# Kernel tuning notes

Hardware: AMD Instinct MI355X
Metric: run time of the kernel (lower is better)

## Reference

```python
import jax, jax.numpy as jnp
import numpy as np

N = 100_000      # n_nodes
E = 1_000_000    # n_edges (avg degree 10)
DIN = 64
DOUT = 64


def setup_inputs() -> dict:
    key = jax.random.key(0)
    k1, k2, k3, k4 = jax.random.split(key, 4)
    x = jax.random.normal(k1, (N, DIN), dtype=jnp.float32)
    edge_index = jax.random.randint(k2, (2, E), 0, N, dtype=jnp.int32)
    # GCNConv linear weight (glorot-ish scale) and bias
    W = jax.random.normal(k3, (DIN, DOUT), dtype=jnp.float32) * (1.0 / np.sqrt(DIN))
    b = jax.random.normal(k4, (DOUT,), dtype=jnp.float32) * 0.01
    return {"x": x, "edge_index": edge_index, "W": W, "b": b}


def reference(x, edge_index, W, b):
    n = x.shape[0]
    # linear transform first (PyG GCNConv: x = self.lin(x))
    h = x @ W  # [N, DOUT]
    # add self-loops
    loop = jnp.arange(n, dtype=edge_index.dtype)
    row = jnp.concatenate([edge_index[0], loop])  # source j
    col = jnp.concatenate([edge_index[1], loop])  # target i
    # symmetric normalization: deg computed on target index (PyG gcn_norm)
    deg = jax.ops.segment_sum(jnp.ones(row.shape[0], dtype=h.dtype), col, num_segments=n)
    dinv = jnp.where(deg > 0, jax.lax.rsqrt(deg), 0.0)
    norm = dinv[row] * dinv[col]  # [E+N]
    # gather source features, scale, scatter-add to targets
    out = jax.ops.segment_sum(norm[:, None] * h[row], col, num_segments=n)
    out = out + b
    # dropout is identity in eval mode; act = relu
    return jax.nn.relu(out)
```

## Files before the change

kernel.cpp:

```cpp
#include <hip/hip_runtime.h>
#include <hip/hip_bf16.h>

#define F 64
#define BK 64
#define CAP 1024
#define ECAP 1024
#define KMAX 1600
#define PA_BLOCKS 512

typedef __attribute__((ext_vector_type(8))) short bf16x8;
typedef __attribute__((ext_vector_type(4))) float f32x4;

static __device__ inline short f2bf_bits(float f) {
    union { __hip_bfloat16 b; short s; } cv;
    cv.b = __float2bfloat16(f);
    return cv.s;
}

__global__ void __launch_bounds__(256)
k1_kernel(const float* __restrict__ x, const float* __restrict__ W,
          __hip_bfloat16* __restrict__ h,
          const int* __restrict__ row, const int* __restrict__ col,
          int* __restrict__ bcursor, unsigned* __restrict__ bin,
          int n, int e, int ngemm, int K, int chunk) {
    __shared__ int smem[2 * KMAX];
    int tid = threadIdx.x;

    if ((int)blockIdx.x < ngemm) {
        short* Wb = (short*)smem;
        for (int i = tid; i < F * F; i += 256) Wb[i] = f2bf_bits(W[i]);
        __syncthreads();
        int lane = tid & 63;
        int wv = tid >> 6;
        int quad = lane >> 4;
        int l16 = lane & 15;

        bf16x8 bfr[2][4];
#pragma unroll
        for (int ks = 0; ks < 2; ++ks)
#pragma unroll
            for (int nb = 0; nb < 4; ++nb) {
                bf16x8 f;
#pragma unroll
                for (int j = 0; j < 8; ++j)
                    f[j] = Wb[(ks * 32 + quad * 8 + j) * F + nb * 16 + l16];
                bfr[ks][nb] = f;
            }

        int blockbase = blockIdx.x * 128;
#pragma unroll
        for (int mt = 0; mt < 2; ++mt) {
            int trow = blockbase + (wv * 2 + mt) * 16;
            int ar = trow + l16;
            bf16x8 af0, af1;
            if (ar < n) {
                const float* xr = x + (size_t)ar * F + quad * 8;
                float4 v0 = ((const float4*)xr)[0];
                float4 v1 = ((const float4*)xr)[1];
                float4 v2 = ((const float4*)(xr + 32))[0];
                float4 v3 = ((const float4*)(xr + 32))[1];
                af0[0] = f2bf_bits(v0.x); af0[1] = f2bf_bits(v0.y);
                af0[2] = f2bf_bits(v0.z); af0[3] = f2bf_bits(v0.w);
                af0[4] = f2bf_bits(v1.x); af0[5] = f2bf_bits(v1.y);
                af0[6] = f2bf_bits(v1.z); af0[7] = f2bf_bits(v1.w);
                af1[0] = f2bf_bits(v2.x); af1[1] = f2bf_bits(v2.y);
                af1[2] = f2bf_bits(v2.z); af1[3] = f2bf_bits(v2.w);
                af1[4] = f2bf_bits(v3.x); af1[5] = f2bf_bits(v3.y);
                af1[6] = f2bf_bits(v3.z); af1[7] = f2bf_bits(v3.w);
            } else {
                af0 = (bf16x8)0; af1 = (bf16x8)0;
            }
            f32x4 acc[4];
#pragma unroll
            for (int nb = 0; nb < 4; ++nb) {
                acc[nb] = (f32x4)0.f;
                acc[nb] = __builtin_amdgcn_mfma_f32_16x16x32_bf16(af0, bfr[0][nb], acc[nb], 0, 0, 0);
                acc[nb] = __builtin_amdgcn_mfma_f32_16x16x32_bf16(af1, bfr[1][nb], acc[nb], 0, 0, 0);
            }
#pragma unroll
            for (int nb = 0; nb < 4; ++nb)
#pragma unroll
                for (int r = 0; r < 4; ++r) {
                    int grow = trow + quad * 4 + r;
                    if (grow < n)
                        h[(size_t)grow * F + nb * 16 + l16] = __float2bfloat16(acc[nb][r]);
                }
        }
    } else {
        int* lh = smem;
        int* lbase = smem + KMAX;
        int pb = blockIdx.x - ngemm;
        int s = pb * chunk;
        int lim = min(s + chunk, e);
        for (int i = tid; i < K; i += 256) lh[i] = 0;
        __syncthreads();
        for (int i = s + tid; i < lim; i += 256) atomicAdd(&lh[col[i] >> 6], 1);
        __syncthreads();
        for (int i = tid; i < K; i += 256) {
            int c = lh[i];
            lbase[i] = c ? atomicAdd(&bcursor[i], c) : 0;
            lh[i] = 0;
        }
        __syncthreads();
        for (int i = s + tid; i < lim; i += 256) {
            int d = col[i];
            int bkt = d >> 6;
            int off = lbase[bkt] + atomicAdd(&lh[bkt], 1);
            if (off < CAP)
                bin[(size_t)bkt * CAP + off] = ((unsigned)row[i] << 6) | ((unsigned)d & 63u);
        }
    }
}

__global__ void __launch_bounds__(256)
dinv_kernel(const unsigned* __restrict__ bin, const int* __restrict__ bcursor,
            float* __restrict__ dinv, int n) {
    __shared__ int lcnt[BK];
    int tid = threadIdx.x;
    int b = blockIdx.x;
    int s = b * CAP;
    int cnt = min(bcursor[b], ECAP);
    if (tid < BK) lcnt[tid] = 0;
    __syncthreads();
    for (int p = tid; p < cnt; p += 256) atomicAdd(&lcnt[bin[s + p] & 63u], 1);
    __syncthreads();
    if (tid < BK) {
        int node = (b << 6) + tid;
        if (node < n) dinv[node] = rsqrtf((float)(lcnt[tid] + 1));
    }
}

__global__ void __launch_bounds__(256)
gather_kernel(const unsigned* __restrict__ bin, const int* __restrict__ bcursor,
              const float* __restrict__ dinv, const __hip_bfloat16* __restrict__ h,
              const float* __restrict__ bias, float* __restrict__ out, int n) {
    __shared__ unsigned ebuf[ECAP];
    __shared__ uint2 sent[ECAP];
    __shared__ int lcnt[BK];
    __shared__ int sstart[BK];
    __shared__ int lcur[BK];
    __shared__ int sc[BK];
    __shared__ float sdinv[BK];
    int tid = threadIdx.x;
    int b = blockIdx.x;
    int base = b << 6;
    int s = b * CAP;
    int cnt = min(bcursor[b], ECAP);

    if (tid < BK) lcnt[tid] = 0;
    __syncthreads();
    for (int p = tid; p < cnt; p += 256) {
        unsigned u = bin[s + p];
        ebuf[p] = u;
        atomicAdd(&lcnt[u & 63u], 1);
    }
    __syncthreads();
    if (tid < BK) sc[tid] = lcnt[tid];
    __syncthreads();
    for (int off = 1; off < BK; off <<= 1) {
        int t = (tid < BK && tid >= off) ? sc[tid - off] : 0;
        __syncthreads();
        if (tid < BK) sc[tid] += t;
        __syncthreads();
    }
    if (tid < BK) {
        int c = lcnt[tid];
        int st = sc[tid] - c;
        sstart[tid] = st;
        lcur[tid] = st;
        sdinv[tid] = rsqrtf((float)(c + 1));
    }
    __syncthreads();
    for (int p = tid; p < cnt; p += 256) {
        unsigned u = ebuf[p];
        int src = (int)(u >> 6);
        float w = dinv[src];
        int pos = atomicAdd(&lcur[u & 63u], 1);
        sent[pos] = make_uint2((unsigned)src, __float_as_uint(w));
    }
    __syncthreads();

    int g = tid >> 3, cl = tid & 7;
    const uint4* h8 = (const uint4*)h;
#pragma unroll
    for (int r = 0; r < 2; ++r) {
        int ln = r * 32 + g;
        int node = base + ln;
        if (node >= n) continue;
        float di = sdinv[ln];
        float a0 = 0.f, a1 = 0.f, a2 = 0.f, a3 = 0.f,
              a4 = 0.f, a5 = 0.f, a6 = 0.f, a7 = 0.f;
        {
            uint4 hv = h8[(size_t)node * 8 + cl];
            a0 = di * __uint_as_float(hv.x << 16);
            a1 = di * __uint_as_float(hv.x & 0xffff0000u);
            a2 = di * __uint_as_float(hv.y << 16);
            a3 = di * __uint_as_float(hv.y & 0xffff0000u);
            a4 = di * __uint_as_float(hv.z << 16);
            a5 = di * __uint_as_float(hv.z & 0xffff0000u);
            a6 = di * __uint_as_float(hv.w << 16);
            a7 = di * __uint_as_float(hv.w & 0xffff0000u);
        }
        int p = sstart[ln];
        int pend = p + lcnt[ln];
        for (; p < pend; ++p) {
            uint2 ew = sent[p];
            float w = __uint_as_float(ew.y);
            uint4 hv = h8[(size_t)ew.x * 8 + cl];
            a0 += w * __uint_as_float(hv.x << 16);
            a1 += w * __uint_as_float(hv.x & 0xffff0000u);
            a2 += w * __uint_as_float(hv.y << 16);
            a3 += w * __uint_as_float(hv.y & 0xffff0000u);
            a4 += w * __uint_as_float(hv.z << 16);
            a5 += w * __uint_as_float(hv.z & 0xffff0000u);
            a6 += w * __uint_as_float(hv.w << 16);
            a7 += w * __uint_as_float(hv.w & 0xffff0000u);
        }
        float4 b0 = ((const float4*)bias)[cl * 2];
        float4 b1 = ((const float4*)bias)[cl * 2 + 1];
        float4 r0, r1;
        r0.x = di * a0 + b0.x; r0.y = di * a1 + b0.y;
        r0.z = di * a2 + b0.z; r0.w = di * a3 + b0.w;
        r1.x = di * a4 + b1.x; r1.y = di * a5 + b1.y;
        r1.z = di * a6 + b1.z; r1.w = di * a7 + b1.w;
        r0.x = r0.x > 0.f ? r0.x : 0.f; r0.y = r0.y > 0.f ? r0.y : 0.f;
        r0.z = r0.z > 0.f ? r0.z : 0.f; r0.w = r0.w > 0.f ? r0.w : 0.f;
        r1.x = r1.x > 0.f ? r1.x : 0.f; r1.y = r1.y > 0.f ? r1.y : 0.f;
        r1.z = r1.z > 0.f ? r1.z : 0.f; r1.w = r1.w > 0.f ? r1.w : 0.f;
        ((float4*)out)[(size_t)node * 16 + cl * 2] = r0;
        ((float4*)out)[(size_t)node * 16 + cl * 2 + 1] = r1;
    }
}

extern "C" void kernel_launch(void* const* d_in, const int* in_sizes, int n_in,
                              void* d_out, int out_size, void* d_ws, size_t ws_size,
                              hipStream_t stream) {
    const float* x = (const float*)d_in[0];
    const int* ei  = (const int*)d_in[1];
    const float* W = (const float*)d_in[2];
    const float* b = (const float*)d_in[3];
    float* out = (float*)d_out;

    int n = in_sizes[0] / F;
    int e = in_sizes[1] / 2;
    const int* row = ei;
    const int* col = ei + e;
    int K = (n + BK - 1) / BK;

    __hip_bfloat16* h = (__hip_bfloat16*)d_ws;
    unsigned* bin = (unsigned*)((char*)d_ws + (size_t)n * F * 2);
    float* dinv   = (float*)(bin + (size_t)KMAX * CAP);
    int* bcursor  = (int*)(dinv + n);

    hipMemsetAsync(bcursor, 0, KMAX * sizeof(int), stream);

    int ngemm = (n + 127) / 128;
    int chunk = (e + PA_BLOCKS - 1) / PA_BLOCKS;
    k1_kernel<<<ngemm + PA_BLOCKS, 256, 0, stream>>>(x, W, h, row, col, bcursor,
                                                     bin, n, e, ngemm, K, chunk);

    dinv_kernel<<<K, 256, 0, stream>>>(bin, bcursor, dinv, n);

    gather_kernel<<<K, 256, 0, stream>>>(bin, bcursor, dinv, h, b, out, n);
}
```

Baseline: 138.7 us.

## Fuse dinv and gather kernels into a cooperative kernel with grid sync

Replaces the separate dinv and gather kernels with one cooperative kernel. Each block handles two 64-node buckets: it loads the edges, computes degrees and dinv, writes dinv to global memory, waits at a grid-wide barrier, then builds the sorted edge list and gathers. This removes one kernel launch and the second read of the bin array. The cost is heavy shared memory use (two sets of buffers), possibly lower occupancy, a grid-sync barrier, and the requirement that all ~782 blocks be co-resident.

```diff
diff --git a/kernel.cpp b/kernel.cpp
--- a/kernel.cpp
+++ b/kernel.cpp
@@ -1,5 +1,8 @@
 #include <hip/hip_runtime.h>
 #include <hip/hip_bf16.h>
+#include <hip/hip_cooperative_groups.h>
+
+namespace cg = cooperative_groups;
 
 #define F 64
 #define BK 64
@@ -112,82 +115,84 @@
     }
 }
 
-__global__ void __launch_bounds__(256)
-dinv_kernel(const unsigned* __restrict__ bin, const int* __restrict__ bcursor,
-            float* __restrict__ dinv, int n) {
-    __shared__ int lcnt[BK];
+__global__ void __launch_bounds__(256, 4)
+fused_kernel(const unsigned* __restrict__ bin, const int* __restrict__ bcursor,
+             float* __restrict__ dinv, const __hip_bfloat16* __restrict__ h,
+             const float* __restrict__ bias, float* __restrict__ out,
+             int n, int K, int nb) {
+    __shared__ unsigned ebuf[2][ECAP];
+    __shared__ uint2 sent[2][ECAP];
+    __shared__ int lcnt[2][BK];
+    __shared__ int sstart[2][BK];
+    __shared__ int lcur[2][BK];
+    __shared__ int sc[2][BK];
+    __shared__ float sdinv[2][BK];
     int tid = threadIdx.x;
-    int b = blockIdx.x;
-    int s = b * CAP;
-    int cnt = min(bcursor[b], ECAP);
-    if (tid < BK) lcnt[tid] = 0;
-    __syncthreads();
-    for (int p = tid; p < cnt; p += 256) atomicAdd(&lcnt[bin[s + p] & 63u], 1);
-    __syncthreads();
-    if (tid < BK) {
-        int node = (b << 6) + tid;
-        if (node < n) dinv[node] = rsqrtf((float)(lcnt[tid] + 1));
-    }
-}
-
-__global__ void __launch_bounds__(256)
-gather_kernel(const unsigned* __restrict__ bin, const int* __restrict__ bcursor,
-              const float* __restrict__ dinv, const __hip_bfloat16* __restrict__ h,
-              const float* __restrict__ bias, float* __restrict__ out, int n) {
-    __shared__ unsigned ebuf[ECAP];
-    __shared__ uint2 sent[ECAP];
-    __shared__ int lcnt[BK];
-    __shared__ int sstart[BK];
-    __shared__ int lcur[BK];
-    __shared__ int sc[BK];
-    __shared__ float sdinv[BK];
-    int tid = threadIdx.x;
-    int b = blockIdx.x;
-    int base = b << 6;
-    int s = b * CAP;
-    int cnt = min(bcursor[b], ECAP);
-
-    if (tid < BK) lcnt[tid] = 0;
-    __syncthreads();
-    for (int p = tid; p < cnt; p += 256) {
-        unsigned u = bin[s + p];
-        ebuf[p] = u;
-        atomicAdd(&lcnt[u & 63u], 1);
-    }
-    __syncthreads();
-    if (tid < BK) sc[tid] = lcnt[tid];
-    __syncthreads();
-    for (int off = 1; off < BK; off <<= 1) {
-        int t = (tid < BK && tid >= off) ? sc[tid - off] : 0;
-        __syncthreads();
-        if (tid < BK) sc[tid] += t;
-        __syncthreads();
-    }
-    if (tid < BK) {
-        int c = lcnt[tid];
-        int st = sc[tid] - c;
-        sstart[tid] = st;
-        lcur[tid] = st;
-        sdinv[tid] = rsqrtf((float)(c + 1));
-    }
-    __syncthreads();
-    for (int p = tid; p < cnt; p += 256) {
-        unsigned u = ebuf[p];
-        int src = (int)(u >> 6);
-        float w = dinv[src];
-        int pos = atomicAdd(&lcur[u & 63u], 1);
-        sent[pos] = make_uint2((unsigned)src, __float_as_uint(w));
+    int b0 = blockIdx.x;
+    int b1 = blockIdx.x + nb;
+    int cntu[2];
+
+    for (int u = 0; u < 2; ++u) {
+        int b = u ? b1 : b0;
+        if (b >= K) { cntu[u] = 0; continue; }
+        int s = b * CAP;
+        int cnt = min(bcursor[b], ECAP);
+        cntu[u] = cnt;
+        if (tid < BK) lcnt[u][tid] = 0;
+        __syncthreads();
+        for (int p = tid; p < cnt; p += 256) {
+            unsigned v = bin[s + p];
+            ebuf[u][p] = v;
+            atomicAdd(&lcnt[u][v & 63u], 1);
+        }
+        __syncthreads();
+        if (tid < BK) sc[u][tid] = lcnt[u][tid];
+        __syncthreads();
+        for (int off = 1; off < BK; off <<= 1) {
+            int t = (tid < BK && tid >= off) ? sc[u][tid - off] : 0;
+            __syncthreads();
+            if (tid < BK) sc[u][tid] += t;
+            __syncthreads();
+        }
+        if (tid < BK) {
+            int c = lcnt[u][tid];
+            int st = sc[u][tid] - c;
+            sstart[u][tid] = st;
+            lcur[u][tid] = st;
+            float dv = rsqrtf((float)(c + 1));
+            sdinv[u][tid] = dv;
+            int node = (b << 6) + tid;
+            if (node < n) dinv[node] = dv;
+        }
+    }
+
+    cg::this_grid().sync();
+
+    for (int u = 0; u < 2; ++u) {
+        int b = u ? b1 : b0;
+        if (b >= K) continue;
+        int cnt = cntu[u];
+        for (int p = tid; p < cnt; p += 256) {
+            unsigned v = ebuf[u][p];
+            int src = (int)(v >> 6);
+            float w = dinv[src];
+            int pos = atomicAdd(&lcur[u][v & 63u], 1);
+            sent[u][pos] = make_uint2((unsigned)src, __float_as_uint(w));
+        }
     }
     __syncthreads();
 
     int g = tid >> 3, cl = tid & 7;
     const uint4* h8 = (const uint4*)h;
 #pragma unroll
-    for (int r = 0; r < 2; ++r) {
-        int ln = r * 32 + g;
-        int node = base + ln;
+    for (int r = 0; r < 4; ++r) {
+        int u = r >> 1;
+        int b = u ? b1 : b0;
+        if (b >= K) continue;
+        int ln = (r & 1) * 32 + g;
+        int node = (b << 6) + ln;
         if (node >= n) continue;
-        float di = sdinv[ln];
+        float di = sdinv[u][ln];
         float a0 = 0.f, a1 = 0.f, a2 = 0.f, a3 = 0.f,
               a4 = 0.f, a5 = 0.f, a6 = 0.f, a7 = 0.f;
         {
@@ -201,10 +206,10 @@
             a6 = di * __uint_as_float(hv.w << 16);
             a7 = di * __uint_as_float(hv.w & 0xffff0000u);
         }
-        int p = sstart[ln];
-        int pend = p + lcnt[ln];
+        int p = sstart[u][ln];
+        int pend = p + lcnt[u][ln];
         for (; p < pend; ++p) {
-            uint2 ew = sent[p];
+            uint2 ew = sent[u][p];
             float w = __uint_as_float(ew.y);
             uint4 hv = h8[(size_t)ew.x * 8 + cl];
             a0 += w * __uint_as_float(hv.x << 16);
@@ -216,13 +221,13 @@
             a6 += w * __uint_as_float(hv.w << 16);
             a7 += w * __uint_as_float(hv.w & 0xffff0000u);
         }
-        float4 b0 = ((const float4*)bias)[cl * 2];
-        float4 b1 = ((const float4*)bias)[cl * 2 + 1];
+        float4 bb0 = ((const float4*)bias)[cl * 2];
+        float4 bb1 = ((const float4*)bias)[cl * 2 + 1];
         float4 r0, r1;
-        r0.x = di * a0 + b0.x; r0.y = di * a1 + b0.y;
-        r0.z = di * a2 + b0.z; r0.w = di * a3 + b0.w;
-        r1.x = di * a4 + b1.x; r1.y = di * a5 + b1.y;
-        r1.z = di * a6 + b1.z; r1.w = di * a7 + b1.w;
+        r0.x = di * a0 + bb0.x; r0.y = di * a1 + bb0.y;
+        r0.z = di * a2 + bb0.z; r0.w = di * a3 + bb0.w;
+        r1.x = di * a4 + bb1.x; r1.y = di * a5 + bb1.y;
+        r1.z = di * a6 + bb1.z; r1.w = di * a7 + bb1.w;
         r0.x = r0.x > 0.f ? r0.x : 0.f; r0.y = r0.y > 0.f ? r0.y : 0.f;
         r0.z = r0.z > 0.f ? r0.z : 0.f; r0.w = r0.w > 0.f ? r0.w : 0.f;
         r1.x = r1.x > 0.f ? r1.x : 0.f; r1.y = r1.y > 0.f ? r1.y : 0.f;
@@ -259,7 +264,8 @@
     k1_kernel<<<ngemm + PA_BLOCKS, 256, 0, stream>>>(x, W, h, row, col, bcursor,
                                                      bin, n, e, ngemm, K, chunk);
 
-    dinv_kernel<<<K, 256, 0, stream>>>(bin, bcursor, dinv, n);
-
-    gather_kernel<<<K, 256, 0, stream>>>(bin, bcursor, dinv, h, b, out, n);
-}
+    int nb = (K + 1) / 2;
+    void* args[] = {(void*)&bin, (void*)&bcursor, (void*)&dinv, (void*)&h,
+                    (void*)&b, (void*)&out, (void*)&n, (void*)&K, (void*)&nb};
+    hipLaunchCooperativeKernel((void*)fused_kernel, dim3(nb), dim3(256), args, 0, stream);
+}
```

Result: slower. 255.7 us (+84.3%).
